# Kernel optimization log

Hardware: AMD Instinct MI355X
Metric: run time of the kernel (lower is better)

## Reference

```python
import jax, jax.numpy as jnp
import numpy as np

B, N, C = 2, 2048, 1024
H = 16
R = 4
MLP = 4096
LORA_SCALE = 1.0 / R  # lora_alpha=1, r=4
EPS = 1e-5


def _ln(x, g, b):
    m = jnp.mean(x, axis=-1, keepdims=True)
    v = jnp.mean(jnp.square(x - m), axis=-1, keepdims=True)
    return (x - m) * jax.lax.rsqrt(v + EPS) * g + b


def setup_inputs() -> dict:
    key = jax.random.key(0)
    ks = jax.random.split(key, 16)
    s = lambda k, shape, fan: jax.random.normal(k, shape, jnp.float32) * (1.0 / np.sqrt(fan))
    return {
        "x": jax.random.normal(ks[0], (B, N, C), jnp.float32),
        "pos": jax.random.normal(ks[1], (B, N, C), jnp.float32),
        "Wqkv": s(ks[2], (3 * C, C), C),
        "b_qkv": jnp.zeros((3 * C,), jnp.float32),
        "lora_A": s(ks[3], (2 * R, C), C),          # rows 0:R -> q, R:2R -> v
        "lora_B": s(ks[4], (2 * C, R), R) * 0.1,     # rows 0:C -> q, C:2C -> v
        "Wproj": s(ks[5], (C, C), C),
        "b_proj": jnp.zeros((C,), jnp.float32),
        "ln1_g": jnp.ones((C,), jnp.float32),
        "ln1_b": jnp.zeros((C,), jnp.float32),
        "ln2_g": jnp.ones((C,), jnp.float32),
        "ln2_b": jnp.zeros((C,), jnp.float32),
        "W1": s(ks[6], (MLP, C), C),
        "b1": jnp.zeros((MLP,), jnp.float32),
        "W2": s(ks[7], (C, MLP), MLP),
        "b2": jnp.zeros((C,), jnp.float32),
        "idx": 0,
    }


def reference(x, pos, Wqkv, b_qkv, lora_A, lora_B, Wproj, b_proj,
              ln1_g, ln1_b, ln2_g, ln2_b, W1, b1, W2, b2, idx):
    # (dropout layers are identity in eval mode)
    x = x + pos

    # --- attention block: Residual(PreNormDrop(SelfAttention)) ---
    h = _ln(x, ln1_g, ln1_b)                              # [B,N,C]
    qkv = h @ Wqkv.T + b_qkv                              # [B,N,3C]
    # LoRA MergedLinear: low-rank update on q and v thirds only
    after_A = h @ lora_A.T                                # [B,N,2R]
    dq = after_A[..., :R] @ lora_B[:C].T * LORA_SCALE     # [B,N,C]
    dv = after_A[..., R:] @ lora_B[C:].T * LORA_SCALE     # [B,N,C]
    qkv = qkv.at[..., :C].add(dq).at[..., 2 * C:].add(dv)

    Dh = C // H
    q, k, v = [t.reshape(B, N, H, Dh).transpose(0, 2, 1, 3)
               for t in jnp.split(qkv, 3, axis=-1)]       # each [B,H,N,Dh]
    scale = Dh ** -0.5
    attn = jnp.einsum('bhid,bhjd->bhij', q, k) * scale    # [B,H,N,N]
    attn = jax.nn.softmax(attn, axis=-1)
    o = jnp.einsum('bhij,bhjd->bhid', attn, v)            # [B,H,N,Dh]
    o = o.transpose(0, 2, 1, 3).reshape(B, N, C)
    o = o @ Wproj.T + b_proj
    x = x + o

    # --- FFN block: Residual(PreNorm(FeedForward)) ---
    h2 = _ln(x, ln2_g, ln2_b)
    h2 = jax.nn.gelu(h2 @ W1.T + b1, approximate=False)
    h2 = h2 @ W2.T + b2
    return x + h2
```

## Files before the change

kernel.cpp:

```cpp
#include <hip/hip_runtime.h>
#include <hip/hip_bf16.h>
#include <math.h>

typedef __hip_bfloat16 bf16;
typedef __attribute__((ext_vector_type(4))) float f32x4;
typedef __attribute__((ext_vector_type(16))) float f32x16;
typedef __attribute__((ext_vector_type(8))) short s16x8;

__device__ __forceinline__ void async_cp16(void* lds, const void* g) {
    __builtin_amdgcn_global_load_lds((const __attribute__((address_space(1))) void*)g,
                                     (__attribute__((address_space(3))) void*)lds, 16, 0, 0);
}

__device__ __forceinline__ float gelu_fast(float x) {
    float y = 1.5957691216f * (x + 0.044715f * x * x * x);
    float t = __expf(y);
    float th = 1.0f - 2.0f / (t + 1.0f);
    return 0.5f * x * (1.0f + th);
}

__global__ __launch_bounds__(256)
void cvt_all(const float* __restrict__ w0, const float* __restrict__ w1,
             const float* __restrict__ w2, const float* __restrict__ w3,
             bf16* __restrict__ o0, bf16* __restrict__ o1,
             bf16* __restrict__ o2, bf16* __restrict__ o3) {
    int i = blockIdx.x * 256 + threadIdx.x;
    const float* src; bf16* dst; int j = i;
    if (j < 786432)            { src = w0; dst = o0; }
    else if (j < 1048576)      { j -= 786432;  src = w1; dst = o1; }
    else if (j < 2097152)      { j -= 1048576; src = w2; dst = o2; }
    else                       { j -= 2097152; src = w3; dst = o3; }
    float4 v = ((const float4*)src)[j];
    union { bf16 o[4]; uint2 u; } pk;
    pk.o[0] = __float2bfloat16(v.x); pk.o[1] = __float2bfloat16(v.y);
    pk.o[2] = __float2bfloat16(v.z); pk.o[3] = __float2bfloat16(v.w);
    ((uint2*)dst)[j] = pk.u;
}

template <bool ADD>
__global__ __launch_bounds__(256)
void ln_kernel(const float* __restrict__ xin, const float* __restrict__ pos,
               const float* __restrict__ gam, const float* __restrict__ bet,
               float* __restrict__ x1, bf16* __restrict__ hout) {
    const int row = blockIdx.x, tid = threadIdx.x;
    const size_t off = (size_t)row * 1024;
    float4 v = ((const float4*)(xin + off))[tid];
    if constexpr (ADD) {
        float4 p = ((const float4*)(pos + off))[tid];
        v.x += p.x; v.y += p.y; v.z += p.z; v.w += p.w;
        ((float4*)(x1 + off))[tid] = v;
    }
    float s  = v.x + v.y + v.z + v.w;
    float s2 = v.x*v.x + v.y*v.y + v.z*v.z + v.w*v.w;
#pragma unroll
    for (int o = 32; o >= 1; o >>= 1) { s += __shfl_xor(s, o); s2 += __shfl_xor(s2, o); }
    __shared__ float sS[4], sS2[4];
    int w = tid >> 6, lane = tid & 63;
    if (lane == 0) { sS[w] = s; sS2[w] = s2; }
    __syncthreads();
    float mean = (sS[0] + sS[1] + sS[2] + sS[3]) * (1.f / 1024.f);
    float e2   = (sS2[0] + sS2[1] + sS2[2] + sS2[3]) * (1.f / 1024.f);
    float rstd = rsqrtf(e2 - mean * mean + 1e-5f);
    float4 gv = ((const float4*)gam)[tid], bv = ((const float4*)bet)[tid];
    bf16* ho = hout + off + tid * 4;
    ho[0] = __float2bfloat16((v.x - mean) * rstd * gv.x + bv.x);
    ho[1] = __float2bfloat16((v.y - mean) * rstd * gv.y + bv.y);
    ho[2] = __float2bfloat16((v.z - mean) * rstd * gv.z + bv.z);
    ho[3] = __float2bfloat16((v.w - mean) * rstd * gv.w + bv.w);
}

template <int MODE>
__global__ __launch_bounds__(256)
void gemm_bk64(const bf16* __restrict__ A, const bf16* __restrict__ B,
               const float* __restrict__ bias, bf16* __restrict__ outp,
               int M, int N, int K, int gx) {
    __shared__ bf16 As[2][128 * 64];
    __shared__ bf16 Bs[2][128 * 64];
    const int tid = threadIdx.x;
    const int lane = tid & 63, w = tid >> 6;
    const int grp = lane >> 4, c16 = lane & 15;
    const int wm = (w & 1) * 64, wn = (w >> 1) * 64;
    const int nwg = gridDim.x, bid = blockIdx.x;
    const int sw = (bid & 7) * (nwg >> 3) + (bid >> 3);
    const int bm = (sw / gx) * 128, bn = (sw % gx) * 128;

    f32x4 acc[4][4];
    const f32x4 zero = {0.f, 0.f, 0.f, 0.f};
#pragma unroll
    for (int mi = 0; mi < 4; mi++)
#pragma unroll
        for (int ni = 0; ni < 4; ni++) acc[mi][ni] = zero;

#define STAGE128(bufi, k0)                                                          \
    {                                                                               \
        const int buf_ = (bufi);                                                    \
        const int koff_ = (k0);                                                     \
        _Pragma("unroll") for (int t_ = 0; t_ < 4; t_++) {                          \
            int s_ = t_ * 256 + tid;                                                \
            int row_ = s_ >> 3, db_ = s_ & 7;                                       \
            int gb_ = (db_ ^ (row_ & 7)) << 3;                                      \
            async_cp16(&As[buf_][s_ * 8], A + (size_t)(bm + row_) * K + koff_ + gb_); \
            async_cp16(&Bs[buf_][s_ * 8], B + (size_t)(bn + row_) * K + koff_ + gb_); \
        }                                                                           \
    }

#define COMPUTE128(bufi)                                                            \
    {                                                                               \
        const int buf_ = (bufi);                                                    \
        _Pragma("unroll") for (int kc_ = 0; kc_ < 2; kc_++) {                       \
            s16x8 af_[4], bfv_[4];                                                  \
            _Pragma("unroll") for (int mi_ = 0; mi_ < 4; mi_++) {                   \
                int r_ = wm + mi_ * 16 + c16;                                       \
                af_[mi_] = *(const s16x8*)&As[buf_][r_ * 64 + ((((kc_ << 2) | grp) ^ (r_ & 7)) << 3)]; \
            }                                                                       \
            _Pragma("unroll") for (int ni_ = 0; ni_ < 4; ni_++) {                   \
                int r_ = wn + ni_ * 16 + c16;                                       \
                bfv_[ni_] = *(const s16x8*)&Bs[buf_][r_ * 64 + ((((kc_ << 2) | grp) ^ (r_ & 7)) << 3)]; \
            }                                                                       \
            _Pragma("unroll") for (int mi_ = 0; mi_ < 4; mi_++)                     \
                _Pragma("unroll") for (int ni_ = 0; ni_ < 4; ni_++)                 \
                    acc[mi_][ni_] = __builtin_amdgcn_mfma_f32_16x16x32_bf16(af_[mi_], bfv_[ni_], acc[mi_][ni_], 0, 0, 0); \
        }                                                                           \
    }

    STAGE128(0, 0);
    __syncthreads();
    const int nk = K >> 6;
    int cur = 0;
    for (int t = 0; t < nk - 1; t++) {
        STAGE128(cur ^ 1, (t + 1) << 6);
        COMPUTE128(cur);
        __syncthreads();
        cur ^= 1;
    }
    COMPUTE128(cur);

#undef STAGE128
#undef COMPUTE128

#pragma unroll
    for (int mi = 0; mi < 4; mi++)
#pragma unroll
        for (int ni = 0; ni < 4; ni++) {
            int r0 = bm + wm + mi * 16 + grp * 4;
            int c  = bn + wn + ni * 16 + c16;
            float bv = bias[c];
#pragma unroll
            for (int q = 0; q < 4; q++) {
                size_t idx = (size_t)(r0 + q) * N + c;
                float v = acc[mi][ni][q] + bv;
                if constexpr (MODE == 2) v = gelu_fast(v);
                outp[idx] = __float2bfloat16(v);
            }
        }
}

__global__ __launch_bounds__(256)
void gemm_n64(const bf16* __restrict__ A, const bf16* __restrict__ B,
              const float* __restrict__ bias, const float* __restrict__ resid,
              float* __restrict__ outp, int M, int N, int K, int gx) {
    __shared__ bf16 As[2][128 * 64];
    __shared__ bf16 Bs[2][64 * 64];
    const int tid = threadIdx.x;
    const int lane = tid & 63, w = tid >> 6;
    const int grp = lane >> 4, c16 = lane & 15;
    const int wm = w * 32;
    const int nwg = gridDim.x, bid = blockIdx.x;
    const int sw = (bid & 7) * (nwg >> 3) + (bid >> 3);
    const int bm = (sw / gx) * 128, bn = (sw % gx) * 64;

    f32x4 acc[2][4];
    const f32x4 zero = {0.f, 0.f, 0.f, 0.f};
#pragma unroll
    for (int mi = 0; mi < 2; mi++)
#pragma unroll
        for (int ni = 0; ni < 4; ni++) acc[mi][ni] = zero;

#define STAGE64(bufi, k0)                                                           \
    {                                                                               \
        const int buf_ = (bufi);                                                    \
        const int koff_ = (k0);                                                     \
        _Pragma("unroll") for (int t_ = 0; t_ < 4; t_++) {                          \
            int s_ = t_ * 256 + tid;                                                \
            int row_ = s_ >> 3, db_ = s_ & 7;                                       \
            async_cp16(&As[buf_][s_ * 8], A + (size_t)(bm + row_) * K + koff_ + ((db_ ^ (row_ & 7)) << 3)); \
        }                                                                           \
        _Pragma("unroll") for (int t_ = 0; t_ < 2; t_++) {                          \
            int s_ = t_ * 256 + tid;                                                \
            int row_ = s_ >> 3, db_ = s_ & 7;                                       \
            async_cp16(&Bs[buf_][s_ * 8], B + (size_t)(bn + row_) * K + koff_ + ((db_ ^ (row_ & 7)) << 3)); \
        }                                                                           \
    }

#define COMPUTE64(bufi)                                                             \
    {                                                                               \
        const int buf_ = (bufi);                                                    \
        _Pragma("unroll") for (int kc_ = 0; kc_ < 2; kc_++) {                       \
            s16x8 af_[2], bfv_[4];                                                  \
            _Pragma("unroll") for (int mi_ = 0; mi_ < 2; mi_++) {                   \
                int r_ = wm + mi_ * 16 + c16;                                       \
                af_[mi_] = *(const s16x8*)&As[buf_][r_ * 64 + ((((kc_ << 2) | grp) ^ (r_ & 7)) << 3)]; \
            }                                                                       \
            _Pragma("unroll") for (int ni_ = 0; ni_ < 4; ni_++) {                   \
                int rb_ = ni_ * 16 + c16;                                           \
                bfv_[ni_] = *(const s16x8*)&Bs[buf_][rb_ * 64 + ((((kc_ << 2) | grp) ^ (rb_ & 7)) << 3)]; \
            }                                                                       \
            _Pragma("unroll") for (int mi_ = 0; mi_ < 2; mi_++)                     \
                _Pragma("unroll") for (int ni_ = 0; ni_ < 4; ni_++)                 \
                    acc[mi_][ni_] = __builtin_amdgcn_mfma_f32_16x16x32_bf16(af_[mi_], bfv_[ni_], acc[mi_][ni_], 0, 0, 0); \
        }                                                                           \
    }

    STAGE64(0, 0);
    __syncthreads();
    const int nk = K >> 6;
    int cur = 0;
    for (int t = 0; t < nk - 1; t++) {
        STAGE64(cur ^ 1, (t + 1) << 6);
        COMPUTE64(cur);
        __syncthreads();
        cur ^= 1;
    }
    COMPUTE64(cur);

#undef STAGE64
#undef COMPUTE64

#pragma unroll
    for (int mi = 0; mi < 2; mi++)
#pragma unroll
        for (int ni = 0; ni < 4; ni++) {
            int r0 = bm + wm + mi * 16 + grp * 4;
            int c  = bn + ni * 16 + c16;
            float bv = bias[c];
#pragma unroll
            for (int q = 0; q < 4; q++) {
                size_t idx = (size_t)(r0 + q) * N + c;
                outp[idx] = acc[mi][ni][q] + bv + resid[idx];
            }
        }
}

__global__ __launch_bounds__(256)
void lora_a_kernel(const bf16* __restrict__ h, const float* __restrict__ A,
                   float* __restrict__ afterA) {
    const int row = blockIdx.x, tid = threadIdx.x;
    float hv[4];
#pragma unroll
    for (int t = 0; t < 4; t++) hv[t] = __bfloat162float(h[(size_t)row * 1024 + tid * 4 + t]);
    float p[8];
#pragma unroll
    for (int r = 0; r < 8; r++) {
        float4 av = ((const float4*)(A + (size_t)r * 1024))[tid];
        p[r] = hv[0] * av.x + hv[1] * av.y + hv[2] * av.z + hv[3] * av.w;
    }
#pragma unroll
    for (int r = 0; r < 8; r++)
#pragma unroll
        for (int o = 32; o >= 1; o >>= 1) p[r] += __shfl_xor(p[r], o);
    __shared__ float red[4][8];
    int w = tid >> 6, lane = tid & 63;
    if (lane == 0) {
#pragma unroll
        for (int r = 0; r < 8; r++) red[w][r] = p[r];
    }
    __syncthreads();
    if (tid < 8) afterA[(size_t)row * 8 + tid] = red[0][tid] + red[1][tid] + red[2][tid] + red[3][tid];
}

__global__ __launch_bounds__(256)
void attn_prep(const bf16* __restrict__ qkv, const float* __restrict__ afterA,
               const float* __restrict__ loraB, bf16* __restrict__ Qb,
               bf16* __restrict__ Kb, bf16* __restrict__ Vt) {
    const int bh = blockIdx.y, b = bh >> 4, h = bh & 15;
    const int it = blockIdx.x;
    __shared__ bf16 Vs[64 * 65];
    const int tid = threadIdx.x;
#pragma unroll
    for (int t = 0; t < 16; t++) {
        int s = t * 256 + tid;
        int il = s >> 6, d = s & 63;
        int ig = b * 2048 + it * 64 + il;
        size_t grow = (size_t)ig * 3072 + h * 64 + d;
        int col = h * 64 + d;
        const float* aA = afterA + (size_t)ig * 8;
        float4 bq = ((const float4*)loraB)[col];
        float4 bvv = ((const float4*)loraB)[1024 + col];
        float dq = (aA[0]*bq.x  + aA[1]*bq.y  + aA[2]*bq.z  + aA[3]*bq.w)  * 0.25f;
        float dv = (aA[4]*bvv.x + aA[5]*bvv.y + aA[6]*bvv.z + aA[7]*bvv.w) * 0.25f;
        float q = (__bfloat162float(qkv[grow]) + dq) * 0.18033688011f;
        float k = __bfloat162float(qkv[grow + 1024]);
        float v = __bfloat162float(qkv[grow + 2048]) + dv;
        size_t orow = (size_t)(bh * 2048 + it * 64 + il) * 64 + d;
        Qb[orow] = __float2bfloat16(q);
        Kb[orow] = __float2bfloat16(k);
        Vs[d * 65 + il] = __float2bfloat16(v);
    }
    __syncthreads();
#pragma unroll
    for (int t = 0; t < 16; t++) {
        int s = t * 256 + tid;
        int d = s >> 6, il = s & 63;
        Vt[(size_t)(bh * 64 + d) * 2048 + it * 64 + il] = Vs[d * 65 + il];
    }
}

__global__ __launch_bounds__(256)
void attn_fused(const bf16* __restrict__ Qb, const bf16* __restrict__ Kb,
                const bf16* __restrict__ Vt, bf16* __restrict__ Og) {
    __shared__ bf16 Qs[128 * 64], Ks[64 * 64], Vs[64 * 64];
    const int tid = threadIdx.x;
    const int lane = tid & 63, w = tid >> 6;
    const int c32 = lane & 31, l5 = lane >> 5;
    const int bh = blockIdx.y, b = bh >> 4, h = bh & 15;
    const int i0 = blockIdx.x * 128;
    const int rowperm = (c32 & 19) | (((c32 >> 3) & 1) << 2) | (((c32 >> 2) & 1) << 3);

    const size_t qbase = (size_t)(bh * 2048 + i0) * 64;
#pragma unroll
    for (int t = 0; t < 4; t++) {
        int s = t * 256 + tid;
        int row = s >> 3, db = s & 7;
        async_cp16(&Qs[s * 8], Qb + qbase + row * 64 + ((db ^ (row & 7)) << 3));
    }
    __syncthreads();
    s16x8 qf[4];
    {
        int rq = w * 32 + c32;
#pragma unroll
        for (int kc = 0; kc < 4; kc++) {
            int db = 2 * kc + l5;
            qf[kc] = *(const s16x8*)&Qs[rq * 64 + ((db ^ (rq & 7)) << 3)];
        }
    }

    f32x16 Oq[2];
#pragma unroll
    for (int dq = 0; dq < 2; dq++)
#pragma unroll
        for (int r = 0; r < 16; r++) Oq[dq][r] = 0.f;
    float l_lane = 0.f;

    for (int j0 = 0; j0 < 2048; j0 += 64) {
        __syncthreads();
#pragma unroll
        for (int t = 0; t < 2; t++) {
            int s = t * 256 + tid;
            int row = s >> 3, db = s & 7;
            int gb = (db ^ (row & 7)) << 3;
            async_cp16(&Ks[s * 8], Kb + (size_t)(bh * 2048 + j0 + row) * 64 + gb);
            async_cp16(&Vs[s * 8], Vt + (size_t)(bh * 64 + row) * 2048 + j0 + gb);
        }
        __syncthreads();

        f32x16 Sq[2];
#pragma unroll
        for (int jq = 0; jq < 2; jq++) {
#pragma unroll
            for (int r = 0; r < 16; r++) Sq[jq][r] = 0.f;
            int rk = jq * 32 + rowperm;
#pragma unroll
            for (int kc = 0; kc < 4; kc++) {
                int db = 2 * kc + l5;
                s16x8 af = *(const s16x8*)&Ks[rk * 64 + ((db ^ (rk & 7)) << 3)];
                Sq[jq] = __builtin_amdgcn_mfma_f32_32x32x16_bf16(af, qf[kc], Sq[jq], 0, 0, 0);
            }
        }

        s16x8 pf[4];
#pragma unroll
        for (int kc = 0; kc < 4; kc++) {
            union { s16x8 v; bf16 e[8]; } u;
#pragma unroll
            for (int jj = 0; jj < 8; jj++) {
                float p = exp2f(Sq[kc >> 1][8 * (kc & 1) + jj]);
                l_lane += p;
                u.e[jj] = __float2bfloat16(p);
            }
            pf[kc] = u.v;
        }

#pragma unroll
        for (int dq = 0; dq < 2; dq++) {
            int rd = dq * 32 + c32;
#pragma unroll
            for (int kc = 0; kc < 4; kc++) {
                int jb = 2 * kc + l5;
                s16x8 af = *(const s16x8*)&Vs[rd * 64 + ((jb ^ (rd & 7)) << 3)];
                Oq[dq] = __builtin_amdgcn_mfma_f32_32x32x16_bf16(af, pf[kc], Oq[dq], 0, 0, 0);
            }
        }
    }

    float l = l_lane + __shfl_xor(l_lane, 32);
    float inv = 1.0f / fmaxf(l, 1e-35f);
    int i = i0 + w * 32 + c32;
    size_t obase = (size_t)(b * 2048 + i) * 1024 + h * 64;
#pragma unroll
    for (int dq = 0; dq < 2; dq++)
#pragma unroll
        for (int rg = 0; rg < 4; rg++) {
            union { bf16 e[4]; uint2 u; } pk;
#pragma unroll
            for (int c = 0; c < 4; c++)
                pk.e[c] = __float2bfloat16(Oq[dq][rg * 4 + c] * inv);
            int d0 = dq * 32 + l5 * 4 + rg * 8;
            *(uint2*)&Og[obase + d0] = pk.u;
        }
}

extern "C" void kernel_launch(void* const* d_in, const int* in_sizes, int n_in,
                              void* d_out, int out_size, void* d_ws, size_t ws_size,
                              hipStream_t stream) {
    const float* x     = (const float*)d_in[0];
    const float* pos   = (const float*)d_in[1];
    const float* Wqkv  = (const float*)d_in[2];
    const float* bqkv  = (const float*)d_in[3];
    const float* loraA = (const float*)d_in[4];
    const float* loraB = (const float*)d_in[5];
    const float* Wproj = (const float*)d_in[6];
    const float* bproj = (const float*)d_in[7];
    const float* ln1g  = (const float*)d_in[8];
    const float* ln1b  = (const float*)d_in[9];
    const float* ln2g  = (const float*)d_in[10];
    const float* ln2b  = (const float*)d_in[11];
    const float* W1    = (const float*)d_in[12];
    const float* b1    = (const float*)d_in[13];
    const float* W2    = (const float*)d_in[14];
    const float* b2    = (const float*)d_in[15];

    char* ws = (char*)d_ws;
    float* x1     = (float*)(ws + 0);
    bf16*  hbuf   = (bf16*) (ws + 16777216);
    bf16*  qkv    = (bf16*) (ws + 25165824);
    bf16*  gbuf   = (bf16*) (ws + 50331648);
    float* afterA = (float*)(ws + 83886080);
    bf16*  Qb     = (bf16*) (ws + 84017152);
    bf16*  Kb     = (bf16*) (ws + 92405760);
    bf16*  Vt     = (bf16*) (ws + 100794368);
    bf16*  Obf    = (bf16*) (ws + 109182976);
    bf16*  Wqkvb  = (bf16*) (ws + 117571584);
    bf16*  Wprojb = (bf16*) (ws + 123863040);
    bf16*  W1b    = (bf16*) (ws + 125960192);
    bf16*  W2b    = (bf16*) (ws + 134348800);

    cvt_all<<<12288, 256, 0, stream>>>(Wqkv, Wproj, W1, W2, Wqkvb, Wprojb, W1b, W2b);

    ln_kernel<true><<<4096, 256, 0, stream>>>(x, pos, ln1g, ln1b, x1, hbuf);

    gemm_bk64<0><<<768, 256, 0, stream>>>(hbuf, Wqkvb, bqkv, qkv, 4096, 3072, 1024, 24);

    lora_a_kernel<<<4096, 256, 0, stream>>>(hbuf, loraA, afterA);

    attn_prep<<<dim3(32, 32), 256, 0, stream>>>(qkv, afterA, loraB, Qb, Kb, Vt);
    attn_fused<<<dim3(16, 32), 256, 0, stream>>>(Qb, Kb, Vt, Obf);

    gemm_n64<<<512, 256, 0, stream>>>(Obf, Wprojb, bproj, x1, x1, 4096, 1024, 1024, 16);

    ln_kernel<false><<<4096, 256, 0, stream>>>(x1, nullptr, ln2g, ln2b, nullptr, hbuf);

    gemm_bk64<2><<<1024, 256, 0, stream>>>(hbuf, W1b, b1, gbuf, 4096, 4096, 1024, 32);

    gemm_n64<<<512, 256, 0, stream>>>(gbuf, W2b, b2, x1, (float*)d_out, 4096, 1024, 4096, 16);

    (void)in_sizes; (void)n_in; (void)out_size; (void)ws_size;
}
```

Before: 412.6 us.

## Double-buffer K/V tiles in attention and swizzle block-to-head mapping

The attention kernel now keeps two K/V shared-memory buffers and issues the async loads for the next 64-key tile before computing on the current one. This replaces the two barriers per iteration with one and lets global loads overlap the MFMA work. The launch is flattened to a 1D grid with a swizzled block index, so that consecutive blocks map to different heads and spread over the chip. LDS use grows by 16 KB per block, which may reduce occupancy.

```diff
diff --git a/kernel.cpp b/kernel.cpp
--- a/kernel.cpp
+++ b/kernel.cpp
@@ -308,22 +308,42 @@
 __global__ __launch_bounds__(256)
 void attn_fused(const bf16* __restrict__ Qb, const bf16* __restrict__ Kb,
                 const bf16* __restrict__ Vt, bf16* __restrict__ Og) {
-    __shared__ bf16 Qs[128 * 64], Ks[64 * 64], Vs[64 * 64];
+    __shared__ bf16 Qs[128 * 64], Ks[2][64 * 64], Vs[2][64 * 64];
     const int tid = threadIdx.x;
     const int lane = tid & 63, w = tid >> 6;
     const int c32 = lane & 31, l5 = lane >> 5;
-    const int bh = blockIdx.y, b = bh >> 4, h = bh & 15;
-    const int i0 = blockIdx.x * 128;
+    const int bid = blockIdx.x;
+    const int sw = (bid & 7) * 64 + (bid >> 3);
+    const int bh = sw >> 4, b = bh >> 4, h = bh & 15;
+    const int i0 = (sw & 15) * 128;
     const int rowperm = (c32 & 19) | (((c32 >> 3) & 1) << 2) | (((c32 >> 2) & 1) << 3);
 
     const size_t qbase = (size_t)(bh * 2048 + i0) * 64;
+    const size_t kbase = (size_t)bh * 2048 * 64;
+    const size_t vbase = (size_t)bh * 64 * 2048;
+
+#define STAGEKV(bufi, jv)                                                           \
+    {                                                                               \
+        const int buf_ = (bufi);                                                    \
+        const int joff_ = (jv);                                                     \
+        _Pragma("unroll") for (int t_ = 0; t_ < 2; t_++) {                          \
+            int s_ = t_ * 256 + tid;                                                \
+            int row_ = s_ >> 3, db_ = s_ & 7;                                       \
+            int gb_ = (db_ ^ (row_ & 7)) << 3;                                      \
+            async_cp16(&Ks[buf_][s_ * 8], Kb + kbase + (size_t)(joff_ + row_) * 64 + gb_); \
+            async_cp16(&Vs[buf_][s_ * 8], Vt + vbase + (size_t)row_ * 2048 + joff_ + gb_); \
+        }                                                                           \
+    }
+
 #pragma unroll
     for (int t = 0; t < 4; t++) {
         int s = t * 256 + tid;
         int row = s >> 3, db = s & 7;
         async_cp16(&Qs[s * 8], Qb + qbase + row * 64 + ((db ^ (row & 7)) << 3));
     }
-    __syncthreads();
+    STAGEKV(0, 0);
+    __syncthreads();
+
     s16x8 qf[4];
     {
         int rq = w * 32 + c32;
@@ -341,17 +361,9 @@
         for (int r = 0; r < 16; r++) Oq[dq][r] = 0.f;
     float l_lane = 0.f;
 
-    for (int j0 = 0; j0 < 2048; j0 += 64) {
-        __syncthreads();
-#pragma unroll
-        for (int t = 0; t < 2; t++) {
-            int s = t * 256 + tid;
-            int row = s >> 3, db = s & 7;
-            int gb = (db ^ (row & 7)) << 3;
-            async_cp16(&Ks[s * 8], Kb + (size_t)(bh * 2048 + j0 + row) * 64 + gb);
-            async_cp16(&Vs[s * 8], Vt + (size_t)(bh * 64 + row) * 2048 + j0 + gb);
-        }
-        __syncthreads();
+    int cur = 0;
+    for (int jt = 0; jt < 32; jt++) {
+        if (jt < 31) STAGEKV(cur ^ 1, (jt + 1) << 6);
 
         f32x16 Sq[2];
 #pragma unroll
@@ -362,7 +374,7 @@
 #pragma unroll
             for (int kc = 0; kc < 4; kc++) {
                 int db = 2 * kc + l5;
-                s16x8 af = *(const s16x8*)&Ks[rk * 64 + ((db ^ (rk & 7)) << 3)];
+                s16x8 af = *(const s16x8*)&Ks[cur][rk * 64 + ((db ^ (rk & 7)) << 3)];
                 Sq[jq] = __builtin_amdgcn_mfma_f32_32x32x16_bf16(af, qf[kc], Sq[jq], 0, 0, 0);
             }
         }
@@ -386,10 +398,13 @@
 #pragma unroll
             for (int kc = 0; kc < 4; kc++) {
                 int jb = 2 * kc + l5;
-                s16x8 af = *(const s16x8*)&Vs[rd * 64 + ((jb ^ (rd & 7)) << 3)];
+                s16x8 af = *(const s16x8*)&Vs[cur][rd * 64 + ((jb ^ (rd & 7)) << 3)];
                 Oq[dq] = __builtin_amdgcn_mfma_f32_32x32x16_bf16(af, pf[kc], Oq[dq], 0, 0, 0);
             }
         }
+
+        __syncthreads();
+        cur ^= 1;
     }
 
     float l = l_lane + __shfl_xor(l_lane, 32);
@@ -407,6 +422,7 @@
             int d0 = dq * 32 + l5 * 4 + rg * 8;
             *(uint2*)&Og[obase + d0] = pk.u;
         }
+#undef STAGEKV
 }
 
 extern "C" void kernel_launch(void* const* d_in, const int* in_sizes, int n_in,
@@ -453,7 +469,7 @@
     lora_a_kernel<<<4096, 256, 0, stream>>>(hbuf, loraA, afterA);
 
     attn_prep<<<dim3(32, 32), 256, 0, stream>>>(qkv, afterA, loraB, Qb, Kb, Vt);
-    attn_fused<<<dim3(16, 32), 256, 0, stream>>>(Qb, Kb, Vt, Obf);
+    attn_fused<<<512, 256, 0, stream>>>(Qb, Kb, Vt, Obf);
 
     gemm_n64<<<512, 256, 0, stream>>>(Obf, Wprojb, bproj, x1, x1, 4096, 1024, 1024, 16);
 
```

Result: no change. 411.5 us (-0.3%).
